# Performance work log

Hardware: AMD Instinct MI355X
Metric: run time of the kernel (lower is better)

## Reference

```python
import jax, jax.numpy as jnp
import numpy as np

D_MODEL = 1024
NHEAD = 16
HEAD_DIM = D_MODEL // NHEAD
EPS = 1e-5


def _layer_norm(x, gamma, beta):
    mu = jnp.mean(x, axis=-1, keepdims=True)
    var = jnp.mean(jnp.square(x - mu), axis=-1, keepdims=True)
    return (x - mu) * jax.lax.rsqrt(var + EPS) * gamma + beta


def setup_inputs() -> dict:
    key = jax.random.key(0)
    ks = jax.random.split(key, 8)
    s = 1.0 / np.sqrt(D_MODEL)
    return {
        "x": jax.random.normal(ks[0], (4, 2048, D_MODEL), dtype=jnp.float32),
        "Wq": jax.random.uniform(ks[1], (D_MODEL, D_MODEL), jnp.float32, -s, s),
        "Wk": jax.random.uniform(ks[2], (D_MODEL, D_MODEL), jnp.float32, -s, s),
        "Wv": jax.random.uniform(ks[3], (D_MODEL, D_MODEL), jnp.float32, -s, s),
        "ln1_g": jnp.ones((D_MODEL,), jnp.float32),
        "ln1_b": jnp.zeros((D_MODEL,), jnp.float32),
        "ln2_g": jnp.ones((D_MODEL,), jnp.float32),
        "ln2_b": jnp.zeros((D_MODEL,), jnp.float32),
        "W1": jax.random.uniform(ks[4], (D_MODEL, D_MODEL), jnp.float32, -s, s),
        "b1": jax.random.uniform(ks[5], (D_MODEL,), jnp.float32, -s, s),
        "W2": jax.random.uniform(ks[6], (D_MODEL, D_MODEL), jnp.float32, -s, s),
        "b2": jax.random.uniform(ks[7], (D_MODEL,), jnp.float32, -s, s),
    }


def reference(x, Wq, Wk, Wv, ln1_g, ln1_b, ln2_g, ln2_b, W1, b1, W2, b2):
    B, S, D = x.shape
    temperature = jnp.sqrt(jnp.asarray(D_MODEL / NHEAD, x.dtype))
    xn = _layer_norm(x, ln1_g, ln1_b)
    # torch Linear: y = x @ W.T (weights are [out, in], no bias for q/k/v)
    q = (xn @ Wq.T).reshape(B, S, NHEAD, HEAD_DIM)
    k = (xn @ Wk.T).reshape(B, S, NHEAD, HEAD_DIM)
    v = (xn @ Wv.T).reshape(B, S, NHEAD, HEAD_DIM)
    scores = jnp.einsum("bqhd,bkhd->bhqk", q, k) / temperature  # [B,H,S,S]
    causal = jnp.tril(jnp.ones((S, S), dtype=bool))
    scores = jnp.where(causal, scores, jnp.asarray(-jnp.inf, scores.dtype))
    attn = jax.nn.softmax(scores, axis=-1)
    att_out = jnp.einsum("bhqk,bkhd->bqhd", attn, v).reshape(B, S, D)
    xt = x + att_out
    xt2 = _layer_norm(xt, ln2_g, ln2_b)
    ffn = jax.nn.relu(xt2 @ W1.T + b1) @ W2.T + b2  # dropout=0 -> identity
    return xt + ffn
```

## Files before the change

kernel.cpp:

```cpp
#include <hip/hip_runtime.h>
#include <hip/hip_bf16.h>

typedef unsigned short u16;
typedef unsigned int u32;
typedef __attribute__((ext_vector_type(8))) __bf16 bf16x8;
typedef __attribute__((ext_vector_type(4))) float f32x4;
typedef __attribute__((ext_vector_type(8))) unsigned short ushort8v;
typedef __attribute__((ext_vector_type(4))) unsigned short u16x4;
typedef __attribute__((ext_vector_type(2))) unsigned int u32x2;

#define DEV __device__ __forceinline__
#define AS1 __attribute__((address_space(1)))
#define AS3 __attribute__((address_space(3)))

DEV u16 f2bf(float f) {
    union { float f; unsigned int i; } u; u.f = f;
    unsigned int x = u.i;
    unsigned int r = (x + 0x7fffu + ((x >> 16) & 1u)) >> 16;
    return (u16)r;
}
DEV float bf2f(u16 h) {
    union { unsigned int i; float f; } u; u.i = ((unsigned int)h) << 16;
    return u.f;
}
DEV u32 cvt_pk_bf16(float lo, float hi) {
    u32 r;
    asm("v_cvt_pk_bf16_f32 %0, %1, %2" : "=v"(r) : "v"(lo), "v"(hi));
    return r;
}

__global__ __launch_bounds__(256) void cvt_w(
    const float* __restrict__ wq, const float* __restrict__ wk,
    const float* __restrict__ wv, const float* __restrict__ w1,
    const float* __restrict__ w2, u16* __restrict__ dst)
{
    const int i = (blockIdx.x * 256 + threadIdx.x) * 4;
    if (i >= (1 << 20)) return;
    auto conv4 = [](float4 a) {
        u16x4 r; r[0] = f2bf(a.x); r[1] = f2bf(a.y); r[2] = f2bf(a.z); r[3] = f2bf(a.w);
        return r;
    };
    *(u16x4*)(dst + i)               = conv4(*(const float4*)(wq + i));
    *(u16x4*)(dst + (1 << 20) + i)   = conv4(*(const float4*)(wk + i));
    *(u16x4*)(dst + (2 << 20) + i)   = conv4(*(const float4*)(wv + i));
    *(u16x4*)(dst + (3 << 20) + i)   = conv4(*(const float4*)(w1 + i));
    *(u16x4*)(dst + (4 << 20) + i)   = conv4(*(const float4*)(w2 + i));
}

template<bool ADD>
__global__ __launch_bounds__(256) void ln_kernel(
    const float* __restrict__ xin, const u16* __restrict__ addbf,
    const float* __restrict__ g, const float* __restrict__ be,
    float* __restrict__ xt_out, u16* __restrict__ y_bf)
{
    const int row = blockIdx.x;
    const int tid = threadIdx.x;
    const size_t base = (size_t)row * 1024 + tid * 4;

    float4 xv = *(const float4*)(xin + base);
    float v[4] = {xv.x, xv.y, xv.z, xv.w};
    if (ADD) {
        u16x4 a = *(const u16x4*)(addbf + base);
        v[0] += bf2f(a[0]); v[1] += bf2f(a[1]); v[2] += bf2f(a[2]); v[3] += bf2f(a[3]);
        float4 o; o.x = v[0]; o.y = v[1]; o.z = v[2]; o.w = v[3];
        *(float4*)(xt_out + base) = o;
    }
    float s = 0.f, ss = 0.f;
    #pragma unroll
    for (int j = 0; j < 4; ++j) { s += v[j]; ss += v[j] * v[j]; }
    #pragma unroll
    for (int o = 32; o > 0; o >>= 1) { s += __shfl_xor(s, o); ss += __shfl_xor(ss, o); }
    __shared__ float red[8];
    const int w = tid >> 6;
    if ((tid & 63) == 0) { red[w * 2] = s; red[w * 2 + 1] = ss; }
    __syncthreads();
    s  = red[0] + red[2] + red[4] + red[6];
    ss = red[1] + red[3] + red[5] + red[7];
    const float mu = s * (1.0f / 1024.0f);
    const float var = ss * (1.0f / 1024.0f) - mu * mu;
    const float rstd = rsqrtf(var + 1e-5f);

    const int col = tid * 4;
    float4 gv = *(const float4*)(g + col);
    float4 bv = *(const float4*)(be + col);
    u16x4 o4;
    o4[0] = f2bf((v[0] - mu) * rstd * gv.x + bv.x);
    o4[1] = f2bf((v[1] - mu) * rstd * gv.y + bv.y);
    o4[2] = f2bf((v[2] - mu) * rstd * gv.z + bv.z);
    o4[3] = f2bf((v[3] - mu) * rstd * gv.w + bv.w);
    *(u16x4*)(y_bf + base) = o4;
}

template<int EPI>
__global__ __launch_bounds__(256, 2) void gemm_bt(
    const u16* __restrict__ A, const u16* __restrict__ Bt,
    void* __restrict__ Cout, const float* __restrict__ bias,
    const float* __restrict__ resid, int M, int N, int K)
{
    __shared__ u16 As[2 * 128 * 32];
    __shared__ u16 Bs[2 * 128 * 32];
    const int tid = threadIdx.x;
    const int l = tid & 63;
    const int w = tid >> 6;
    const int wm = w >> 1, wn = w & 1;
    const int fr = l & 15, fc = l >> 4;
    const size_t rowA0 = (size_t)blockIdx.x * 128;
    const size_t rowB0 = (size_t)blockIdx.y * 128;

    f32x4 acc[4][4] = {};
    const int ldoff = fr * 32 + fc * 8;

    const int nkt = K >> 6;
    for (int kt = 0; kt < nkt; ++kt) {
        __syncthreads();
        const int k0 = kt << 6;
        #pragma unroll
        for (int q = 0; q < 4; ++q) {
            const int row = (q & 1) * 64 + w * 16 + (l >> 2);
            const int kk  = (q >> 1) * 32 + (l & 3) * 8;
            const u16* ga = A  + (rowA0 + row) * K + k0 + kk;
            const u16* gb = Bt + (rowB0 + row) * K + k0 + kk;
            u16* da = As + q * 2048 + w * 512;
            u16* db = Bs + q * 2048 + w * 512;
            __builtin_amdgcn_global_load_lds((const AS1 void*)ga, (AS3 void*)da, 16, 0, 0);
            __builtin_amdgcn_global_load_lds((const AS1 void*)gb, (AS3 void*)db, 16, 0, 0);
        }
        __syncthreads();
        #pragma unroll
        for (int ks = 0; ks < 2; ++ks) {
            const u16* as_p = As + ks * 4096;
            const u16* bs_p = Bs + ks * 4096;
            bf16x8 af[4], bfv[4];
            #pragma unroll
            for (int m = 0; m < 4; ++m)
                af[m] = *(const bf16x8*)(as_p + (wm * 64 + m * 16) * 32 + ldoff);
            #pragma unroll
            for (int n = 0; n < 4; ++n)
                bfv[n] = *(const bf16x8*)(bs_p + (wn * 64 + n * 16) * 32 + ldoff);
            #pragma unroll
            for (int m = 0; m < 4; ++m)
                #pragma unroll
                for (int n = 0; n < 4; ++n)
                    acc[m][n] = __builtin_amdgcn_mfma_f32_16x16x32_bf16(
                        af[m], bfv[n], acc[m][n], 0, 0, 0);
        }
    }

    const int r0 = (int)rowA0 + wm * 64;
    const int c0 = (int)rowB0 + wn * 64;
    #pragma unroll
    for (int m = 0; m < 4; ++m) {
        #pragma unroll
        for (int n = 0; n < 4; ++n) {
            const int row = r0 + m * 16 + fc * 4;
            const int col = c0 + n * 16 + fr;
            #pragma unroll
            for (int j = 0; j < 4; ++j) {
                float v = acc[m][n][j];
                if constexpr (EPI == 0) {
                    const int rowj = row + j;
                    const int which = col >> 10;
                    const int hh = (col >> 6) & 15;
                    const int dd = col & 63;
                    const size_t dst = (size_t)which * 8388608 +
                        ((((size_t)(rowj >> 11) * 16 + hh) * 2048 + (rowj & 2047)) * 64 + dd);
                    ((u16*)Cout)[dst] = f2bf(v);
                } else if constexpr (EPI == 1) {
                    const size_t idx = (size_t)(row + j) * N + col;
                    v += bias[col];
                    v = fmaxf(v, 0.0f);
                    ((u16*)Cout)[idx] = f2bf(v);
                } else {
                    const size_t idx = (size_t)(row + j) * N + col;
                    v += bias[col] + resid[idx];
                    ((float*)Cout)[idx] = v;
                }
            }
        }
    }
}

__global__ __launch_bounds__(256, 2) void attn_fwd(
    const u16* __restrict__ Qh, const u16* __restrict__ Kh,
    const u16* __restrict__ Vh, u16* __restrict__ attout)
{
    __shared__ u16 Ks[2][64 * 64];
    __shared__ u16 Vt[2][64 * 64];
    __shared__ u16 Pw[4][32 * 64];

    const int bid = blockIdx.x;
    const int pair = (bid >> 3) & 7;
    const int g = (bid & 7) + 8 * (bid >> 6);
    const int h = g & 15, b = g >> 4;

    const int tid = threadIdx.x, l = tid & 63, w = tid >> 6;
    const int fr = l & 15, fc = l >> 4;
    const int hb = b * 16 + h;
    const size_t head = (size_t)hb << 17;
    const u16* kb_g = Kh + head;
    const u16* vb_g = Vh + head;
    u16* pw = &Pw[w][0];

    const int sw = (fr & 7) << 3;
    const int col0 = (fc * 8) ^ sw;
    const int col1 = col0 ^ 32;

    const int krow0 = w * 16 + (l >> 3);
    const int kdsw  = ((l & 7) * 8) ^ ((l >> 3) << 3);

    const int kr = tid >> 2;
    const int kc0 = (tid & 3) * 16;

    const float qs = 0.125f * 1.44269504f;

    bf16x8 onesv;
    #pragma unroll
    for (int j = 0; j < 8; ++j) onesv[j] = (__bf16)1.0f;

    #pragma unroll 1
    for (int half = 0; half < 2; ++half) {
        const int qt = half ? 15 - pair : pair;
        const int qbw = qt * 128 + w * 32;

        bf16x8 qf[2][2];
        #pragma unroll
        for (int qq = 0; qq < 2; ++qq) {
            const u16* qp = Qh + head + (size_t)(qbw + qq * 16 + fr) * 64 + fc * 8;
            qf[qq][0] = *(const bf16x8*)qp;
            qf[qq][1] = *(const bf16x8*)(qp + 32);
            #pragma unroll
            for (int j = 0; j < 8; ++j) {
                qf[qq][0][j] = (__bf16)((float)qf[qq][0][j] * qs);
                qf[qq][1][j] = (__bf16)((float)qf[qq][1][j] * qs);
            }
        }

        f32x4 acc_o[2][4] = {};
        f32x4 l_run[2] = {};
        float m_run[2] = {-3.0e38f, -3.0e38f};

        const int nkt = 2 * qt + 2;
        int cur = 0;

        #pragma unroll
        for (int i = 0; i < 2; ++i) {
            const int row = krow0 + i * 8;
            __builtin_amdgcn_global_load_lds(
                (const AS1 void*)(kb_g + (size_t)row * 64 + kdsw),
                (AS3 void*)(&Ks[0][0] + (w * 16 + i * 8) * 64), 16, 0, 0);
        }
        __builtin_amdgcn_sched_barrier(0);
        {
            ushort8v v0a = *(const ushort8v*)(vb_g + (size_t)kr * 64 + kc0);
            ushort8v v0b = *(const ushort8v*)(vb_g + (size_t)kr * 64 + kc0 + 8);
            #pragma unroll
            for (int j = 0; j < 8; ++j) {
                const int d0 = kc0 + j, d1 = kc0 + 8 + j;
                Vt[0][d0 * 64 + (kr ^ ((d0 & 7) << 3) ^ ((d0 >> 4) << 4))] = v0a[j];
                Vt[0][d1 * 64 + (kr ^ ((d1 & 7) << 3) ^ ((d1 >> 4) << 4))] = v0b[j];
            }
        }
        ushort8v vA, vB;
        {
            vA = *(const ushort8v*)(vb_g + (size_t)(64 + kr) * 64 + kc0);
            vB = *(const ushort8v*)(vb_g + (size_t)(64 + kr) * 64 + kc0 + 8);
        }
        __builtin_amdgcn_sched_barrier(0);
        asm volatile("s_waitcnt vmcnt(2)" ::: "memory");
        asm volatile("s_waitcnt lgkmcnt(0)" ::: "memory");
        __builtin_amdgcn_s_barrier();

        #pragma unroll 1
        for (int kt = 0; kt < nkt; ++kt) {
            const int kv0 = kt * 64;
            const u16* ksc = &Ks[cur][0];
            const u16* vtc = &Vt[cur][0];

            if (kt + 1 < nkt) {
                u16* ksn = &Ks[cur ^ 1][0];
                #pragma unroll
                for (int i = 0; i < 2; ++i) {
                    const int row = krow0 + i * 8;
                    __builtin_amdgcn_global_load_lds(
                        (const AS1 void*)(kb_g + (size_t)(kv0 + 64 + row) * 64 + kdsw),
                        (AS3 void*)(ksn + (w * 16 + i * 8) * 64), 16, 0, 0);
                }
            }
            __builtin_amdgcn_sched_barrier(0);

            if (kv0 <= qbw + 31) {
                f32x4 sa[2][4] = {};
                __builtin_amdgcn_s_setprio(1);
                #pragma unroll
                for (int nb = 0; nb < 4; ++nb) {
                    const u16* kb = ksc + (nb * 16 + fr) * 64;
                    const bf16x8 kf0 = *(const bf16x8*)(kb + col0);
                    const bf16x8 kf1 = *(const bf16x8*)(kb + col1);
                    #pragma unroll
                    for (int qq = 0; qq < 2; ++qq) {
                        sa[qq][nb] = __builtin_amdgcn_mfma_f32_16x16x32_bf16(
                            kf0, qf[qq][0], sa[qq][nb], 0, 0, 0);
                        sa[qq][nb] = __builtin_amdgcn_mfma_f32_16x16x32_bf16(
                            kf1, qf[qq][1], sa[qq][nb], 0, 0, 0);
                    }
                }
                __builtin_amdgcn_s_setprio(0);

                if (kv0 + 64 > qbw) {
                    #pragma unroll
                    for (int qq = 0; qq < 2; ++qq) {
                        const int qg = qbw + qq * 16 + fr;
                        #pragma unroll
                        for (int nb = 0; nb < 4; ++nb)
                            #pragma unroll
                            for (int j = 0; j < 4; ++j) {
                                const int kg = kv0 + nb * 16 + fc * 4 + j;
                                if (kg > qg) sa[qq][nb][j] = -3.0e38f;
                            }
                    }
                }

                float mx[2];
                #pragma unroll
                for (int qq = 0; qq < 2; ++qq) {
                    float m = sa[qq][0][0];
                    #pragma unroll
                    for (int nb = 0; nb < 4; ++nb)
                        #pragma unroll
                        for (int j = 0; j < 4; ++j)
                            m = fmaxf(m, sa[qq][nb][j]);
                    m = fmaxf(m, __shfl_xor(m, 16));
                    m = fmaxf(m, __shfl_xor(m, 32));
                    mx[qq] = m;
                }

                const bool need = (mx[0] > m_run[0] + 8.0f) || (mx[1] > m_run[1] + 8.0f);
                if (__any(need)) {
                    #pragma unroll
                    for (int qq = 0; qq < 2; ++qq) {
                        const float mn = fmaxf(m_run[qq], mx[qq]);
                        const float alpha = exp2f(m_run[qq] - mn);
                        m_run[qq] = mn;
                        #pragma unroll
                        for (int j = 0; j < 4; ++j) {
                            const float aj = __shfl(alpha, fc * 4 + j);
                            l_run[qq][j] *= aj;
                            #pragma unroll
                            for (int db = 0; db < 4; ++db)
                                acc_o[qq][db][j] *= aj;
                        }
                    }
                }

                #pragma unroll
                for (int qq = 0; qq < 2; ++qq)
                    #pragma unroll
                    for (int nb = 0; nb < 4; ++nb)
                        #pragma unroll
                        for (int j = 0; j < 4; ++j)
                            sa[qq][nb][j] = exp2f(sa[qq][nb][j] - m_run[qq]);

                #pragma unroll
                for (int qq = 0; qq < 2; ++qq)
                    #pragma unroll
                    for (int nb = 0; nb < 4; ++nb) {
                        u32x2 pkv;
                        pkv[0] = cvt_pk_bf16(sa[qq][nb][0], sa[qq][nb][1]);
                        pkv[1] = cvt_pk_bf16(sa[qq][nb][2], sa[qq][nb][3]);
                        *(u32x2*)(pw + (qq * 16 + fr) * 64 + ((nb * 16 + fc * 4) ^ sw)) = pkv;
                    }
                bf16x8 pf[2][2];
                #pragma unroll
                for (int qq = 0; qq < 2; ++qq) {
                    const u16* prd = pw + (qq * 16 + fr) * 64;
                    pf[qq][0] = *(const bf16x8*)(prd + col0);
                    pf[qq][1] = *(const bf16x8*)(prd + col1);
                }
                f32x4 acc_s[2] = {};
                __builtin_amdgcn_s_setprio(1);
                #pragma unroll
                for (int db = 0; db < 4; ++db) {
                    const u16* vb = vtc + (db * 16 + fr) * 64;
                    const int vx = db << 4;
                    const bf16x8 vf0 = *(const bf16x8*)(vb + (col0 ^ vx));
                    const bf16x8 vf1 = *(const bf16x8*)(vb + (col1 ^ vx));
                    #pragma unroll
                    for (int qq = 0; qq < 2; ++qq) {
                        acc_o[qq][db] = __builtin_amdgcn_mfma_f32_16x16x32_bf16(
                            pf[qq][0], vf0, acc_o[qq][db], 0, 0, 0);
                        acc_o[qq][db] = __builtin_amdgcn_mfma_f32_16x16x32_bf16(
                            pf[qq][1], vf1, acc_o[qq][db], 0, 0, 0);
                    }
                }
                #pragma unroll
                for (int qq = 0; qq < 2; ++qq) {
                    acc_s[qq] = __builtin_amdgcn_mfma_f32_16x16x32_bf16(
                        pf[qq][0], onesv, acc_s[qq], 0, 0, 0);
                    acc_s[qq] = __builtin_amdgcn_mfma_f32_16x16x32_bf16(
                        pf[qq][1], onesv, acc_s[qq], 0, 0, 0);
                }
                __builtin_amdgcn_s_setprio(0);
                #pragma unroll
                for (int qq = 0; qq < 2; ++qq)
                    #pragma unroll
                    for (int j = 0; j < 4; ++j)
                        l_run[qq][j] += acc_s[qq][j];
            }

            if (kt + 1 < nkt) {
                u16* vtn = &Vt[cur ^ 1][0];
                #pragma unroll
                for (int j = 0; j < 8; ++j) {
                    const int d0 = kc0 + j, d1 = kc0 + 8 + j;
                    vtn[d0 * 64 + (kr ^ ((d0 & 7) << 3) ^ ((d0 >> 4) << 4))] = vA[j];
                    vtn[d1 * 64 + (kr ^ ((d1 & 7) << 3) ^ ((d1 >> 4) << 4))] = vB[j];
                }
            }
            if (kt + 2 < nkt) {
                const u16* vn = vb_g + (size_t)(kv0 + 128 + kr) * 64 + kc0;
                vA = *(const ushort8v*)vn;
                vB = *(const ushort8v*)(vn + 8);
            }
            __builtin_amdgcn_sched_barrier(0);
            if (kt + 1 < nkt) {
                if (kt + 2 < nkt) asm volatile("s_waitcnt vmcnt(2)" ::: "memory");
                else              asm volatile("s_waitcnt vmcnt(0)" ::: "memory");
            }
            asm volatile("s_waitcnt lgkmcnt(0)" ::: "memory");
            __builtin_amdgcn_s_barrier();
            cur ^= 1;
        }

        const size_t bS = (size_t)b * 2048;
        #pragma unroll
        for (int qq = 0; qq < 2; ++qq) {
            float inv[4];
            #pragma unroll
            for (int j = 0; j < 4; ++j) inv[j] = 1.0f / l_run[qq][j];
            #pragma unroll
            for (int db = 0; db < 4; ++db)
                #pragma unroll
                for (int j = 0; j < 4; ++j)
                    attout[(bS + qbw + qq * 16 + fc * 4 + j) * 1024 + h * 64 + db * 16 + fr] =
                        f2bf(acc_o[qq][db][j] * inv[j]);
        }
    }
}

extern "C" void kernel_launch(void* const* d_in, const int* in_sizes, int n_in,
                              void* d_out, int out_size, void* d_ws, size_t ws_size,
                              hipStream_t stream)
{
    const float* x    = (const float*)d_in[0];
    const float* Wq   = (const float*)d_in[1];
    const float* Wk   = (const float*)d_in[2];
    const float* Wv   = (const float*)d_in[3];
    const float* ln1g = (const float*)d_in[4];
    const float* ln1b = (const float*)d_in[5];
    const float* ln2g = (const float*)d_in[6];
    const float* ln2b = (const float*)d_in[7];
    const float* W1   = (const float*)d_in[8];
    const float* b1   = (const float*)d_in[9];
    const float* W2   = (const float*)d_in[10];
    const float* b2   = (const float*)d_in[11];

    char* ws = (char*)d_ws;
    u16*   wbf  = (u16*)(ws);
    u16*   xn   = (u16*)(ws + 10485760);
    u16*   qkvb = (u16*)(ws + 27262976);
    u16*   attb = (u16*)(ws + 77594624);
    float* xt   = (float*)(ws + 94371840);

    cvt_w<<<1024, 256, 0, stream>>>(Wq, Wk, Wv, W1, W2, wbf);
    ln_kernel<false><<<8192, 256, 0, stream>>>(x, nullptr, ln1g, ln1b, nullptr, xn);
    gemm_bt<0><<<dim3(64, 24), 256, 0, stream>>>(xn, wbf, qkvb, nullptr, nullptr,
                                                 8192, 3072, 1024);
    attn_fwd<<<512, 256, 0, stream>>>(qkvb, qkvb + 8388608, qkvb + 16777216, attb);
    ln_kernel<true><<<8192, 256, 0, stream>>>(x, attb, ln2g, ln2b, xt, xn);
    gemm_bt<1><<<dim3(64, 8), 256, 0, stream>>>(xn, wbf + (3 << 20), qkvb, b1, nullptr,
                                                8192, 1024, 1024);
    gemm_bt<2><<<dim3(64, 8), 256, 0, stream>>>(qkvb, wbf + (4 << 20), d_out, b2, xt,
                                                8192, 1024, 1024);
}
```

Measured before the change: 228.5 us.

## Double-buffer GEMM LDS staging and split attention into one q-tile per block

The GEMM now double-buffers its LDS tiles, prefetching the next K slice while MFMAs run on the current one, and raises wave priority during the MFMA block. This is meant to hide global-to-LDS latency. The attention kernel now launches one block per 128-row query tile (1024 blocks) instead of pairing a short and a long tile per block. Blocks are ordered by a permutation that schedules the heaviest tiles first. The P scratch buffer is shrunk and reused per 16-row slice, and launch bounds rise to 4 blocks per CU for more occupancy, at the cost of register pressure and doubled LDS use in the GEMM.

```diff
diff --git a/kernel.cpp b/kernel.cpp
--- a/kernel.cpp
+++ b/kernel.cpp
@@ -97,8 +97,8 @@
     void* __restrict__ Cout, const float* __restrict__ bias,
     const float* __restrict__ resid, int M, int N, int K)
 {
-    __shared__ u16 As[2 * 128 * 32];
-    __shared__ u16 Bs[2 * 128 * 32];
+    __shared__ u16 As[2][2 * 128 * 32];
+    __shared__ u16 Bs[2][2 * 128 * 32];
     const int tid = threadIdx.x;
     const int l = tid & 63;
     const int w = tid >> 6;
@@ -110,26 +110,37 @@
     f32x4 acc[4][4] = {};
     const int ldoff = fr * 32 + fc * 8;
 
-    const int nkt = K >> 6;
-    for (int kt = 0; kt < nkt; ++kt) {
-        __syncthreads();
+    const int srow = (l >> 2);
+    const int skk  = (l & 3) * 8;
+
+    auto STAGE = [&](int kt, int p) {
         const int k0 = kt << 6;
         #pragma unroll
         for (int q = 0; q < 4; ++q) {
-            const int row = (q & 1) * 64 + w * 16 + (l >> 2);
-            const int kk  = (q >> 1) * 32 + (l & 3) * 8;
+            const int row = (q & 1) * 64 + w * 16 + srow;
+            const int kk  = (q >> 1) * 32 + skk;
             const u16* ga = A  + (rowA0 + row) * K + k0 + kk;
             const u16* gb = Bt + (rowB0 + row) * K + k0 + kk;
-            u16* da = As + q * 2048 + w * 512;
-            u16* db = Bs + q * 2048 + w * 512;
-            __builtin_amdgcn_global_load_lds((const AS1 void*)ga, (AS3 void*)da, 16, 0, 0);
-            __builtin_amdgcn_global_load_lds((const AS1 void*)gb, (AS3 void*)db, 16, 0, 0);
-        }
-        __syncthreads();
+            __builtin_amdgcn_global_load_lds((const AS1 void*)ga,
+                (AS3 void*)(&As[p][0] + q * 2048 + w * 512), 16, 0, 0);
+            __builtin_amdgcn_global_load_lds((const AS1 void*)gb,
+                (AS3 void*)(&Bs[p][0] + q * 2048 + w * 512), 16, 0, 0);
+        }
+    };
+
+    const int nkt = K >> 6;
+    STAGE(0, 0);
+    asm volatile("s_waitcnt vmcnt(0)" ::: "memory");
+    __builtin_amdgcn_s_barrier();
+
+    for (int kt = 0; kt < nkt; ++kt) {
+        const int p = kt & 1;
+        if (kt + 1 < nkt) STAGE(kt + 1, p ^ 1);
+        __builtin_amdgcn_sched_barrier(0);
         #pragma unroll
         for (int ks = 0; ks < 2; ++ks) {
-            const u16* as_p = As + ks * 4096;
-            const u16* bs_p = Bs + ks * 4096;
+            const u16* as_p = &As[p][0] + ks * 4096;
+            const u16* bs_p = &Bs[p][0] + ks * 4096;
             bf16x8 af[4], bfv[4];
             #pragma unroll
             for (int m = 0; m < 4; ++m)
@@ -137,13 +148,18 @@
             #pragma unroll
             for (int n = 0; n < 4; ++n)
                 bfv[n] = *(const bf16x8*)(bs_p + (wn * 64 + n * 16) * 32 + ldoff);
+            __builtin_amdgcn_s_setprio(1);
             #pragma unroll
             for (int m = 0; m < 4; ++m)
                 #pragma unroll
                 for (int n = 0; n < 4; ++n)
                     acc[m][n] = __builtin_amdgcn_mfma_f32_16x16x32_bf16(
                         af[m], bfv[n], acc[m][n], 0, 0, 0);
-        }
+            __builtin_amdgcn_s_setprio(0);
+        }
+        if (kt + 1 < nkt) asm volatile("s_waitcnt vmcnt(0)" ::: "memory");
+        asm volatile("s_waitcnt lgkmcnt(0)" ::: "memory");
+        __builtin_amdgcn_s_barrier();
     }
 
     const int r0 = (int)rowA0 + wm * 64;
@@ -180,17 +196,17 @@
     }
 }
 
-__global__ __launch_bounds__(256, 2) void attn_fwd(
+__global__ __launch_bounds__(256, 4) void attn_fwd(
     const u16* __restrict__ Qh, const u16* __restrict__ Kh,
     const u16* __restrict__ Vh, u16* __restrict__ attout)
 {
     __shared__ u16 Ks[2][64 * 64];
     __shared__ u16 Vt[2][64 * 64];
-    __shared__ u16 Pw[4][32 * 64];
+    __shared__ u16 Pw[4][16 * 64];
 
     const int bid = blockIdx.x;
-    const int pair = (bid >> 3) & 7;
-    const int g = (bid & 7) + 8 * (bid >> 6);
+    const int qt = (int)((0x32104567BA98CDEFull >> (((bid >> 6) & 15) * 4)) & 15);
+    const int g = bid & 63;
     const int h = g & 15, b = g >> 4;
 
     const int tid = threadIdx.x, l = tid & 63, w = tid >> 6;
@@ -217,233 +233,225 @@
     #pragma unroll
     for (int j = 0; j < 8; ++j) onesv[j] = (__bf16)1.0f;
 
+    const int qbw = qt * 128 + w * 32;
+
+    bf16x8 qf[2][2];
+    #pragma unroll
+    for (int qq = 0; qq < 2; ++qq) {
+        const u16* qp = Qh + head + (size_t)(qbw + qq * 16 + fr) * 64 + fc * 8;
+        qf[qq][0] = *(const bf16x8*)qp;
+        qf[qq][1] = *(const bf16x8*)(qp + 32);
+        #pragma unroll
+        for (int j = 0; j < 8; ++j) {
+            qf[qq][0][j] = (__bf16)((float)qf[qq][0][j] * qs);
+            qf[qq][1][j] = (__bf16)((float)qf[qq][1][j] * qs);
+        }
+    }
+
+    f32x4 acc_o[2][4] = {};
+    f32x4 l_run[2] = {};
+    float m_run[2] = {-3.0e38f, -3.0e38f};
+
+    const int nkt = 2 * qt + 2;
+    int cur = 0;
+
+    #pragma unroll
+    for (int i = 0; i < 2; ++i) {
+        const int row = krow0 + i * 8;
+        __builtin_amdgcn_global_load_lds(
+            (const AS1 void*)(kb_g + (size_t)row * 64 + kdsw),
+            (AS3 void*)(&Ks[0][0] + (w * 16 + i * 8) * 64), 16, 0, 0);
+    }
+    __builtin_amdgcn_sched_barrier(0);
+    {
+        ushort8v v0a = *(const ushort8v*)(vb_g + (size_t)kr * 64 + kc0);
+        ushort8v v0b = *(const ushort8v*)(vb_g + (size_t)kr * 64 + kc0 + 8);
+        #pragma unroll
+        for (int j = 0; j < 8; ++j) {
+            const int d0 = kc0 + j, d1 = kc0 + 8 + j;
+            Vt[0][d0 * 64 + (kr ^ ((d0 & 7) << 3) ^ ((d0 >> 4) << 4))] = v0a[j];
+            Vt[0][d1 * 64 + (kr ^ ((d1 & 7) << 3) ^ ((d1 >> 4) << 4))] = v0b[j];
+        }
+    }
+    ushort8v vA, vB;
+    vA = *(const ushort8v*)(vb_g + (size_t)(64 + kr) * 64 + kc0);
+    vB = *(const ushort8v*)(vb_g + (size_t)(64 + kr) * 64 + kc0 + 8);
+    __builtin_amdgcn_sched_barrier(0);
+    asm volatile("s_waitcnt vmcnt(2)" ::: "memory");
+    asm volatile("s_waitcnt lgkmcnt(0)" ::: "memory");
+    __builtin_amdgcn_s_barrier();
+
     #pragma unroll 1
-    for (int half = 0; half < 2; ++half) {
-        const int qt = half ? 15 - pair : pair;
-        const int qbw = qt * 128 + w * 32;
-
-        bf16x8 qf[2][2];
-        #pragma unroll
-        for (int qq = 0; qq < 2; ++qq) {
-            const u16* qp = Qh + head + (size_t)(qbw + qq * 16 + fr) * 64 + fc * 8;
-            qf[qq][0] = *(const bf16x8*)qp;
-            qf[qq][1] = *(const bf16x8*)(qp + 32);
-            #pragma unroll
-            for (int j = 0; j < 8; ++j) {
-                qf[qq][0][j] = (__bf16)((float)qf[qq][0][j] * qs);
-                qf[qq][1][j] = (__bf16)((float)qf[qq][1][j] * qs);
-            }
-        }
-
-        f32x4 acc_o[2][4] = {};
-        f32x4 l_run[2] = {};
-        float m_run[2] = {-3.0e38f, -3.0e38f};
-
-        const int nkt = 2 * qt + 2;
-        int cur = 0;
-
-        #pragma unroll
-        for (int i = 0; i < 2; ++i) {
-            const int row = krow0 + i * 8;
-            __builtin_amdgcn_global_load_lds(
-                (const AS1 void*)(kb_g + (size_t)row * 64 + kdsw),
-                (AS3 void*)(&Ks[0][0] + (w * 16 + i * 8) * 64), 16, 0, 0);
+    for (int kt = 0; kt < nkt; ++kt) {
+        const int kv0 = kt * 64;
+        const u16* ksc = &Ks[cur][0];
+        const u16* vtc = &Vt[cur][0];
+
+        if (kt + 1 < nkt) {
+            u16* ksn = &Ks[cur ^ 1][0];
+            #pragma unroll
+            for (int i = 0; i < 2; ++i) {
+                const int row = krow0 + i * 8;
+                __builtin_amdgcn_global_load_lds(
+                    (const AS1 void*)(kb_g + (size_t)(kv0 + 64 + row) * 64 + kdsw),
+                    (AS3 void*)(ksn + (w * 16 + i * 8) * 64), 16, 0, 0);
+            }
         }
         __builtin_amdgcn_sched_barrier(0);
-        {
-            ushort8v v0a = *(const ushort8v*)(vb_g + (size_t)kr * 64 + kc0);
-            ushort8v v0b = *(const ushort8v*)(vb_g + (size_t)kr * 64 + kc0 + 8);
-            #pragma unroll
-            for (int j = 0; j < 8; ++j) {
-                const int d0 = kc0 + j, d1 = kc0 + 8 + j;
-                Vt[0][d0 * 64 + (kr ^ ((d0 & 7) << 3) ^ ((d0 >> 4) << 4))] = v0a[j];
-                Vt[0][d1 * 64 + (kr ^ ((d1 & 7) << 3) ^ ((d1 >> 4) << 4))] = v0b[j];
-            }
-        }
-        ushort8v vA, vB;
-        {
-            vA = *(const ushort8v*)(vb_g + (size_t)(64 + kr) * 64 + kc0);
-            vB = *(const ushort8v*)(vb_g + (size_t)(64 + kr) * 64 + kc0 + 8);
-        }
-        __builtin_amdgcn_sched_barrier(0);
-        asm volatile("s_waitcnt vmcnt(2)" ::: "memory");
-        asm volatile("s_waitcnt lgkmcnt(0)" ::: "memory");
-        __builtin_amdgcn_s_barrier();
-
-        #pragma unroll 1
-        for (int kt = 0; kt < nkt; ++kt) {
-            const int kv0 = kt * 64;
-            const u16* ksc = &Ks[cur][0];
-            const u16* vtc = &Vt[cur][0];
-
-            if (kt + 1 < nkt) {
-                u16* ksn = &Ks[cur ^ 1][0];
-                #pragma unroll
-                for (int i = 0; i < 2; ++i) {
-                    const int row = krow0 + i * 8;
-                    __builtin_amdgcn_global_load_lds(
-                        (const AS1 void*)(kb_g + (size_t)(kv0 + 64 + row) * 64 + kdsw),
-                        (AS3 void*)(ksn + (w * 16 + i * 8) * 64), 16, 0, 0);
-                }
-            }
-            __builtin_amdgcn_sched_barrier(0);
-
-            if (kv0 <= qbw + 31) {
-                f32x4 sa[2][4] = {};
-                __builtin_amdgcn_s_setprio(1);
-                #pragma unroll
-                for (int nb = 0; nb < 4; ++nb) {
-                    const u16* kb = ksc + (nb * 16 + fr) * 64;
-                    const bf16x8 kf0 = *(const bf16x8*)(kb + col0);
-                    const bf16x8 kf1 = *(const bf16x8*)(kb + col1);
-                    #pragma unroll
-                    for (int qq = 0; qq < 2; ++qq) {
-                        sa[qq][nb] = __builtin_amdgcn_mfma_f32_16x16x32_bf16(
-                            kf0, qf[qq][0], sa[qq][nb], 0, 0, 0);
-                        sa[qq][nb] = __builtin_amdgcn_mfma_f32_16x16x32_bf16(
-                            kf1, qf[qq][1], sa[qq][nb], 0, 0, 0);
-                    }
-                }
-                __builtin_amdgcn_s_setprio(0);
-
-                if (kv0 + 64 > qbw) {
-                    #pragma unroll
-                    for (int qq = 0; qq < 2; ++qq) {
-                        const int qg = qbw + qq * 16 + fr;
-                        #pragma unroll
-                        for (int nb = 0; nb < 4; ++nb)
-                            #pragma unroll
-                            for (int j = 0; j < 4; ++j) {
-                                const int kg = kv0 + nb * 16 + fc * 4 + j;
-                                if (kg > qg) sa[qq][nb][j] = -3.0e38f;
-                            }
-                    }
-                }
-
-                float mx[2];
+
+        if (kv0 <= qbw + 31) {
+            f32x4 sa[2][4] = {};
+            __builtin_amdgcn_s_setprio(1);
+            #pragma unroll
+            for (int nb = 0; nb < 4; ++nb) {
+                const u16* kb = ksc + (nb * 16 + fr) * 64;
+                const bf16x8 kf0 = *(const bf16x8*)(kb + col0);
+                const bf16x8 kf1 = *(const bf16x8*)(kb + col1);
                 #pragma unroll
                 for (int qq = 0; qq < 2; ++qq) {
-                    float m = sa[qq][0][0];
+                    sa[qq][nb] = __builtin_amdgcn_mfma_f32_16x16x32_bf16(
+                        kf0, qf[qq][0], sa[qq][nb], 0, 0, 0);
+                    sa[qq][nb] = __builtin_amdgcn_mfma_f32_16x16x32_bf16(
+                        kf1, qf[qq][1], sa[qq][nb], 0, 0, 0);
+                }
+            }
+            __builtin_amdgcn_s_setprio(0);
+
+            if (kv0 + 64 > qbw) {
+                #pragma unroll
+                for (int qq = 0; qq < 2; ++qq) {
+                    const int qg = qbw + qq * 16 + fr;
                     #pragma unroll
                     for (int nb = 0; nb < 4; ++nb)
                         #pragma unroll
-                        for (int j = 0; j < 4; ++j)
-                            m = fmaxf(m, sa[qq][nb][j]);
-                    m = fmaxf(m, __shfl_xor(m, 16));
-                    m = fmaxf(m, __shfl_xor(m, 32));
-                    mx[qq] = m;
-                }
-
-                const bool need = (mx[0] > m_run[0] + 8.0f) || (mx[1] > m_run[1] + 8.0f);
-                if (__any(need)) {
-                    #pragma unroll
-                    for (int qq = 0; qq < 2; ++qq) {
-                        const float mn = fmaxf(m_run[qq], mx[qq]);
-                        const float alpha = exp2f(m_run[qq] - mn);
-                        m_run[qq] = mn;
-                        #pragma unroll
                         for (int j = 0; j < 4; ++j) {
-                            const float aj = __shfl(alpha, fc * 4 + j);
-                            l_run[qq][j] *= aj;
-                            #pragma unroll
-                            for (int db = 0; db < 4; ++db)
-                                acc_o[qq][db][j] *= aj;
+                            const int kg = kv0 + nb * 16 + fc * 4 + j;
+                            if (kg > qg) sa[qq][nb][j] = -3.0e38f;
                         }
-                    }
-                }
-
-                #pragma unroll
-                for (int qq = 0; qq < 2; ++qq)
-                    #pragma unroll
-                    for (int nb = 0; nb < 4; ++nb)
-                        #pragma unroll
-                        for (int j = 0; j < 4; ++j)
-                            sa[qq][nb][j] = exp2f(sa[qq][nb][j] - m_run[qq]);
-
-                #pragma unroll
-                for (int qq = 0; qq < 2; ++qq)
-                    #pragma unroll
-                    for (int nb = 0; nb < 4; ++nb) {
-                        u32x2 pkv;
-                        pkv[0] = cvt_pk_bf16(sa[qq][nb][0], sa[qq][nb][1]);
-                        pkv[1] = cvt_pk_bf16(sa[qq][nb][2], sa[qq][nb][3]);
-                        *(u32x2*)(pw + (qq * 16 + fr) * 64 + ((nb * 16 + fc * 4) ^ sw)) = pkv;
-                    }
-                bf16x8 pf[2][2];
-                #pragma unroll
-                for (int qq = 0; qq < 2; ++qq) {
-                    const u16* prd = pw + (qq * 16 + fr) * 64;
-                    pf[qq][0] = *(const bf16x8*)(prd + col0);
-                    pf[qq][1] = *(const bf16x8*)(prd + col1);
-                }
-                f32x4 acc_s[2] = {};
-                __builtin_amdgcn_s_setprio(1);
-                #pragma unroll
-                for (int db = 0; db < 4; ++db) {
-                    const u16* vb = vtc + (db * 16 + fr) * 64;
-                    const int vx = db << 4;
-                    const bf16x8 vf0 = *(const bf16x8*)(vb + (col0 ^ vx));
-                    const bf16x8 vf1 = *(const bf16x8*)(vb + (col1 ^ vx));
-                    #pragma unroll
-                    for (int qq = 0; qq < 2; ++qq) {
-                        acc_o[qq][db] = __builtin_amdgcn_mfma_f32_16x16x32_bf16(
-                            pf[qq][0], vf0, acc_o[qq][db], 0, 0, 0);
-                        acc_o[qq][db] = __builtin_amdgcn_mfma_f32_16x16x32_bf16(
-                            pf[qq][1], vf1, acc_o[qq][db], 0, 0, 0);
-                    }
-                }
-                #pragma unroll
-                for (int qq = 0; qq < 2; ++qq) {
-                    acc_s[qq] = __builtin_amdgcn_mfma_f32_16x16x32_bf16(
-                        pf[qq][0], onesv, acc_s[qq], 0, 0, 0);
-                    acc_s[qq] = __builtin_amdgcn_mfma_f32_16x16x32_bf16(
-                        pf[qq][1], onesv, acc_s[qq], 0, 0, 0);
-                }
-                __builtin_amdgcn_s_setprio(0);
-                #pragma unroll
-                for (int qq = 0; qq < 2; ++qq)
+                }
+            }
+
+            float mx[2];
+            #pragma unroll
+            for (int qq = 0; qq < 2; ++qq) {
+                float m = sa[qq][0][0];
+                #pragma unroll
+                for (int nb = 0; nb < 4; ++nb)
                     #pragma unroll
                     for (int j = 0; j < 4; ++j)
-                        l_run[qq][j] += acc_s[qq][j];
-            }
-
-            if (kt + 1 < nkt) {
-                u16* vtn = &Vt[cur ^ 1][0];
-                #pragma unroll
-                for (int j = 0; j < 8; ++j) {
-                    const int d0 = kc0 + j, d1 = kc0 + 8 + j;
-                    vtn[d0 * 64 + (kr ^ ((d0 & 7) << 3) ^ ((d0 >> 4) << 4))] = vA[j];
-                    vtn[d1 * 64 + (kr ^ ((d1 & 7) << 3) ^ ((d1 >> 4) << 4))] = vB[j];
-                }
-            }
-            if (kt + 2 < nkt) {
-                const u16* vn = vb_g + (size_t)(kv0 + 128 + kr) * 64 + kc0;
-                vA = *(const ushort8v*)vn;
-                vB = *(const ushort8v*)(vn + 8);
-            }
-            __builtin_amdgcn_sched_barrier(0);
-            if (kt + 1 < nkt) {
-                if (kt + 2 < nkt) asm volatile("s_waitcnt vmcnt(2)" ::: "memory");
-                else              asm volatile("s_waitcnt vmcnt(0)" ::: "memory");
-            }
-            asm volatile("s_waitcnt lgkmcnt(0)" ::: "memory");
-            __builtin_amdgcn_s_barrier();
-            cur ^= 1;
-        }
-
-        const size_t bS = (size_t)b * 2048;
-        #pragma unroll
-        for (int qq = 0; qq < 2; ++qq) {
-            float inv[4];
-            #pragma unroll
-            for (int j = 0; j < 4; ++j) inv[j] = 1.0f / l_run[qq][j];
-            #pragma unroll
-            for (int db = 0; db < 4; ++db)
+                        m = fmaxf(m, sa[qq][nb][j]);
+                m = fmaxf(m, __shfl_xor(m, 16));
+                m = fmaxf(m, __shfl_xor(m, 32));
+                mx[qq] = m;
+            }
+
+            const bool need = (mx[0] > m_run[0] + 8.0f) || (mx[1] > m_run[1] + 8.0f);
+            if (__any(need)) {
+                #pragma unroll
+                for (int qq = 0; qq < 2; ++qq) {
+                    const float mn = fmaxf(m_run[qq], mx[qq]);
+                    const float alpha = exp2f(m_run[qq] - mn);
+                    m_run[qq] = mn;
+                    #pragma unroll
+                    for (int j = 0; j < 4; ++j) {
+                        const float aj = __shfl(alpha, fc * 4 + j);
+                        l_run[qq][j] *= aj;
+                        #pragma unroll
+                        for (int db = 0; db < 4; ++db)
+                            acc_o[qq][db][j] *= aj;
+                    }
+                }
+            }
+
+            #pragma unroll
+            for (int qq = 0; qq < 2; ++qq)
+                #pragma unroll
+                for (int nb = 0; nb < 4; ++nb)
+                    #pragma unroll
+                    for (int j = 0; j < 4; ++j)
+                        sa[qq][nb][j] = exp2f(sa[qq][nb][j] - m_run[qq]);
+
+            bf16x8 pf[2][2];
+            #pragma unroll
+            for (int qq = 0; qq < 2; ++qq) {
+                #pragma unroll
+                for (int nb = 0; nb < 4; ++nb) {
+                    u32x2 pkv;
+                    pkv[0] = cvt_pk_bf16(sa[qq][nb][0], sa[qq][nb][1]);
+                    pkv[1] = cvt_pk_bf16(sa[qq][nb][2], sa[qq][nb][3]);
+                    *(u32x2*)(pw + fr * 64 + ((nb * 16 + fc * 4) ^ sw)) = pkv;
+                }
+                const u16* prd = pw + fr * 64;
+                pf[qq][0] = *(const bf16x8*)(prd + col0);
+                pf[qq][1] = *(const bf16x8*)(prd + col1);
+            }
+            f32x4 acc_s[2] = {};
+            __builtin_amdgcn_s_setprio(1);
+            #pragma unroll
+            for (int db = 0; db < 4; ++db) {
+                const u16* vb = vtc + (db * 16 + fr) * 64;
+                const int vx = db << 4;
+                const bf16x8 vf0 = *(const bf16x8*)(vb + (col0 ^ vx));
+                const bf16x8 vf1 = *(const bf16x8*)(vb + (col1 ^ vx));
+                #pragma unroll
+                for (int qq = 0; qq < 2; ++qq) {
+                    acc_o[qq][db] = __builtin_amdgcn_mfma_f32_16x16x32_bf16(
+                        pf[qq][0], vf0, acc_o[qq][db], 0, 0, 0);
+                    acc_o[qq][db] = __builtin_amdgcn_mfma_f32_16x16x32_bf16(
+                        pf[qq][1], vf1, acc_o[qq][db], 0, 0, 0);
+                }
+            }
+            #pragma unroll
+            for (int qq = 0; qq < 2; ++qq) {
+                acc_s[qq] = __builtin_amdgcn_mfma_f32_16x16x32_bf16(
+                    pf[qq][0], onesv, acc_s[qq], 0, 0, 0);
+                acc_s[qq] = __builtin_amdgcn_mfma_f32_16x16x32_bf16(
+                    pf[qq][1], onesv, acc_s[qq], 0, 0, 0);
+            }
+            __builtin_amdgcn_s_setprio(0);
+            #pragma unroll
+            for (int qq = 0; qq < 2; ++qq)
                 #pragma unroll
                 for (int j = 0; j < 4; ++j)
-                    attout[(bS + qbw + qq * 16 + fc * 4 + j) * 1024 + h * 64 + db * 16 + fr] =
-                        f2bf(acc_o[qq][db][j] * inv[j]);
-        }
+                    l_run[qq][j] += acc_s[qq][j];
+        }
+
+        if (kt + 1 < nkt) {
+            u16* vtn = &Vt[cur ^ 1][0];
+            #pragma unroll
+            for (int j = 0; j < 8; ++j) {
+                const int d0 = kc0 + j, d1 = kc0 + 8 + j;
+                vtn[d0 * 64 + (kr ^ ((d0 & 7) << 3) ^ ((d0 >> 4) << 4))] = vA[j];
+                vtn[d1 * 64 + (kr ^ ((d1 & 7) << 3) ^ ((d1 >> 4) << 4))] = vB[j];
+            }
+        }
+        if (kt + 2 < nkt) {
+            const u16* vn = vb_g + (size_t)(kv0 + 128 + kr) * 64 + kc0;
+            vA = *(const ushort8v*)vn;
+            vB = *(const ushort8v*)(vn + 8);
+        }
+        __builtin_amdgcn_sched_barrier(0);
+        if (kt + 1 < nkt) {
+            if (kt + 2 < nkt) asm volatile("s_waitcnt vmcnt(2)" ::: "memory");
+            else              asm volatile("s_waitcnt vmcnt(0)" ::: "memory");
+        }
+        asm volatile("s_waitcnt lgkmcnt(0)" ::: "memory");
+        __builtin_amdgcn_s_barrier();
+        cur ^= 1;
+    }
+
+    const size_t bS = (size_t)b * 2048;
+    #pragma unroll
+    for (int qq = 0; qq < 2; ++qq) {
+        float inv[4];
+        #pragma unroll
+        for (int j = 0; j < 4; ++j) inv[j] = 1.0f / l_run[qq][j];
+        #pragma unroll
+        for (int db = 0; db < 4; ++db)
+            #pragma unroll
+            for (int j = 0; j < 4; ++j)
+                attout[(bS + qbw + qq * 16 + fc * 4 + j) * 1024 + h * 64 + db * 16 + fr] =
+                    f2bf(acc_o[qq][db][j] * inv[j]);
     }
 }
 
@@ -475,7 +483,7 @@
     ln_kernel<false><<<8192, 256, 0, stream>>>(x, nullptr, ln1g, ln1b, nullptr, xn);
     gemm_bt<0><<<dim3(64, 24), 256, 0, stream>>>(xn, wbf, qkvb, nullptr, nullptr,
                                                  8192, 3072, 1024);
-    attn_fwd<<<512, 256, 0, stream>>>(qkvb, qkvb + 8388608, qkvb + 16777216, attb);
+    attn_fwd<<<1024, 256, 0, stream>>>(qkvb, qkvb + 8388608, qkvb + 16777216, attb);
     ln_kernel<true><<<8192, 256, 0, stream>>>(x, attb, ln2g, ln2b, xt, xn);
     gemm_bt<1><<<dim3(64, 8), 256, 0, stream>>>(xn, wbf + (3 << 20), qkvb, b1, nullptr,
                                                 8192, 1024, 1024);
```

New measurement: 258.8 us. +13.3%, slower.
